# Kernel tuning notes

Measured on AMD Instinct MI355X. Metric: run time of the kernel, lower is better.

## Reference

```python
import jax, jax.numpy as jnp
import numpy as np

BS, SEQ, D, H = 2, 2048, 1024, 16
HD = D // H  # head_dim = 64


def setup_inputs() -> dict:
    key = jax.random.key(0)
    kx, kw = jax.random.split(key)
    x = jax.random.normal(kx, (BS, SEQ, D), dtype=jnp.float32)
    # qkv Linear: weight [3D, D] (xavier_normal), bias zeros
    std = float(np.sqrt(2.0 / (D + 3 * D)))
    W_qkv = jax.random.normal(kw, (3 * D, D), dtype=jnp.float32) * std
    b_qkv = jnp.zeros((3 * D,), dtype=jnp.float32)
    return {"x": x, "W_qkv": W_qkv, "b_qkv": b_qkv}


def reference(x, W_qkv, b_qkv):
    bs, seq_len, embed_dim = x.shape
    # fused QKV projection: [bs, seq, 3D]
    qkv = x @ W_qkv.T + b_qkv
    qkv = qkv.reshape(bs, seq_len, 3, H, HD)
    qkv = jnp.transpose(qkv, (2, 0, 3, 1, 4))  # [3, bs, H, seq, HD]
    Q, K, V = qkv[0], qkv[1], qkv[2]
    # past_kv is None -> total_len == seq_len, past_len == 0
    scores = jnp.einsum("bhqd,bhkd->bhqk", Q, K) / jnp.sqrt(jnp.float32(HD))
    # causal mask: True above diagonal -> -inf
    mask = jnp.triu(jnp.ones((seq_len, seq_len), dtype=bool), k=1)
    scores = jnp.where(mask[None, None, :, :], -jnp.inf, scores)
    probs = jax.nn.softmax(scores, axis=-1)
    # attn_dropout = 0.0 (eval) -> identity
    out = jnp.einsum("bhqk,bhkd->bhqd", probs, V)
    out = jnp.transpose(out, (0, 2, 1, 3)).reshape(bs, seq_len, embed_dim)
    return (out, (K, V))
```

## Files before the change

### kernel.cpp

```cpp
#include <hip/hip_runtime.h>

typedef __bf16 bf16_t;
typedef __bf16 bf16x8 __attribute__((ext_vector_type(8)));
typedef float f32x4 __attribute__((ext_vector_type(4)));
typedef unsigned long long u64;

__device__ __forceinline__ unsigned short bfbits(float f) {
  unsigned u = __float_as_uint(f);
  u += 0x7fffu + ((u >> 16) & 1u);
  return (unsigned short)(u >> 16);
}
__device__ __forceinline__ bf16_t f2bf(float f) {
  unsigned short s = bfbits(f);
  union { unsigned short s; bf16_t b; } cv; cv.s = s; return cv.b;
}

__device__ __forceinline__ void gl16(const void* g, void* l) {
  __builtin_amdgcn_global_load_lds(
      (const __attribute__((address_space(1))) void*)g,
      (__attribute__((address_space(3))) void*)l,
      16, 0, 0);
}

__global__ __launch_bounds__(256) void cvt_kernel(const float* __restrict__ x,
                                                  const float* __restrict__ Wf,
                                                  bf16_t* __restrict__ xb,
                                                  bf16_t* __restrict__ wb) {
  const int i = blockIdx.x * 256 + threadIdx.x;
  const float* src; bf16_t* dst; int j;
  if (i < 524288) { j = i; src = x; dst = xb; }
  else            { j = i - 524288; src = Wf; dst = wb; }
  const float4* s = (const float4*)src + (size_t)j * 2;
  float4 a = s[0], b = s[1];
  bf16x8 o;
  o[0] = f2bf(a.x); o[1] = f2bf(a.y); o[2] = f2bf(a.z); o[3] = f2bf(a.w);
  o[4] = f2bf(b.x); o[5] = f2bf(b.y); o[6] = f2bf(b.z); o[7] = f2bf(b.w);
  const int row = j >> 7, jr = j & 127;
  const int dstc = (row << 7) + (jr & ~3) + ((jr & 3) ^ ((row >> 1) & 3));
  *((bf16x8*)dst + dstc) = o;
}

#define GEMM_K 1024
__global__ __launch_bounds__(256) void qkv_gemm(
    const bf16_t* __restrict__ A,
    const bf16_t* __restrict__ B,
    const float* __restrict__ bias,
    float* __restrict__ Ko, float* __restrict__ Vo,
    bf16_t* __restrict__ Qb, bf16_t* __restrict__ Kb,
    bf16_t* __restrict__ Vt,
    int* __restrict__ qcnt)
{
  if (blockIdx.x == 0 && threadIdx.x == 0) *qcnt = 0;
  __shared__ bf16_t lsA[128 * 32];
  __shared__ bf16_t lsB[128 * 32];
  const int tid = threadIdx.x;
  const int lane = tid & 63;
  const int ln = lane & 15, qd = lane >> 4;
  const int wid = tid >> 6;
  const int wm = wid & 1, wn = wid >> 1;
  const int bm = blockIdx.x & 31, bn = blockIdx.x >> 5;
  const int m0 = bm * 128, n0 = bn * 128;
  const int qs = qd ^ ((ln >> 1) & 3);

  f32x4 acc[4][4] = {};

  const int c0 = tid, c1 = tid + 256;
  const bf16_t* ga0 = A + (size_t)(m0 + (c0 >> 2)) * GEMM_K + (c0 & 3) * 8;
  const bf16_t* ga1 = A + (size_t)(m0 + (c1 >> 2)) * GEMM_K + (c1 & 3) * 8;
  const bf16_t* gb0 = B + (size_t)(n0 + (c0 >> 2)) * GEMM_K + (c0 & 3) * 8;
  const bf16_t* gb1 = B + (size_t)(n0 + (c1 >> 2)) * GEMM_K + (c1 & 3) * 8;
  bf16_t* la0 = &lsA[c0 * 8];
  bf16_t* la1 = &lsA[c1 * 8];
  bf16_t* lb0 = &lsB[c0 * 8];
  bf16_t* lb1 = &lsB[c1 * 8];

  for (int k0 = 0; k0 < GEMM_K; k0 += 32) {
    __syncthreads();
    gl16(ga0 + k0, la0);
    gl16(ga1 + k0, la1);
    gl16(gb0 + k0, lb0);
    gl16(gb1 + k0, lb1);
    __syncthreads();
    bf16x8 af[4], bf[4];
#pragma unroll
    for (int mi = 0; mi < 4; ++mi)
      af[mi] = *(const bf16x8*)&lsA[(wm * 64 + mi * 16 + ln) * 32 + qs * 8];
#pragma unroll
    for (int ni = 0; ni < 4; ++ni)
      bf[ni] = *(const bf16x8*)&lsB[(wn * 64 + ni * 16 + ln) * 32 + qs * 8];
#pragma unroll
    for (int mi = 0; mi < 4; ++mi)
#pragma unroll
      for (int ni = 0; ni < 4; ++ni)
        acc[mi][ni] = __builtin_amdgcn_mfma_f32_16x16x32_bf16(af[mi], bf[ni], acc[mi][ni], 0, 0, 0);
  }

  const int sec = n0 >> 10;
#pragma unroll
  for (int mi = 0; mi < 4; ++mi) {
#pragma unroll
    for (int ni = 0; ni < 4; ++ni) {
      const int colg = n0 + wn * 64 + ni * 16 + ln;
      const float bv = bias[colg];
      const int cc = colg & 1023, h = cc >> 6, hd = cc & 63;
#pragma unroll
      for (int r = 0; r < 4; ++r) {
        const int mg = m0 + wm * 64 + mi * 16 + qd * 4 + r;
        const int b = mg >> 11, s = mg & 2047;
        const float val = acc[mi][ni][r] + bv;
        const int bhi = b * 16 + h;
        const size_t pidx = ((size_t)(bhi * 2048 + s)) * 64 + hd;
        const size_t sidx = (size_t)bhi * 131072 + (size_t)(s >> 6) * 4096 +
                            (size_t)(s & 63) * 64 + (((hd >> 3) ^ (s & 7)) << 3) + (hd & 7);
        if (sec == 0) {
          Qb[sidx] = f2bf(val * 0.18033688f);
        } else if (sec == 1) {
          Ko[pidx] = val;
          Kb[sidx] = f2bf(val);
        } else {
          Vo[pidx] = val;
          const size_t vidx = (size_t)bhi * 131072 + (size_t)(s >> 6) * 4096 +
                              (size_t)hd * 64 + ((((s >> 3) & 7) ^ (hd & 7)) << 3) + (s & 7);
          Vt[vidx] = f2bf(val);
        }
      }
    }
  }
}

__global__ __launch_bounds__(256) void attn_kernel(
    const bf16_t* __restrict__ Qb,
    const bf16_t* __restrict__ Kb,
    const bf16_t* __restrict__ Vt,
    float* __restrict__ Out,
    int* __restrict__ qcnt)
{
  __shared__ bf16_t lq[8192];
  __shared__ bf16_t lk[8192];
  __shared__ bf16_t lv[8192];
  __shared__ bf16_t lp[8192];
  __shared__ int task_sh;
  const int tid = threadIdx.x;
  const int lane = tid & 63, ln = lane & 15, qd = lane >> 4;
  const int w = tid >> 6;
  const int l7 = ln & 7;

  for (;;) {
    __syncthreads();
    if (tid == 0) task_sh = atomicAdd(qcnt, 1);
    __syncthreads();
    const int task = task_sh;
    if (task >= 512) break;
    const int it = (task < 256) ? (15 - (task >> 5)) : ((task - 256) >> 5);
    const int bh = task & 31;
    const int b = bh >> 4, h = bh & 15;

    const bf16_t* qbase = Qb + (size_t)bh * 131072 + (size_t)it * 8192;
    const bf16_t* kbase = Kb + (size_t)bh * 131072;
    const bf16_t* vbase = Vt + (size_t)bh * 131072;

#pragma unroll
    for (int i = 0; i < 4; ++i) {
      const int cc = tid + i * 256;
      gl16(qbase + cc * 8, &lq[cc * 8]);
      gl16(kbase + cc * 8, &lk[cc * 8]);
      gl16(vbase + cc * 8, &lv[cc * 8]);
    }
    __syncthreads();

    bf16x8 afq[2][2];
#pragma unroll
    for (int kk = 0; kk < 2; ++kk)
#pragma unroll
      for (int qi = 0; qi < 2; ++qi) {
        const int row = w * 32 + qi * 16 + ln;
        afq[kk][qi] = *(const bf16x8*)&lq[(row >> 6) * 4096 + (row & 63) * 64 +
                                          (((kk * 4 + qd) ^ l7) << 3)];
      }

    f32x4 oc[2][4] = {};
    float lsum[2] = {0.f, 0.f};
    const int qg = it * 128 + w * 32 + ln;

    for (int st = 0; st <= it; ++st) {
      if (st > 0) {
        __syncthreads();
#pragma unroll
        for (int i = 0; i < 4; ++i) {
          const int cc = tid + i * 256;
          gl16(kbase + (size_t)st * 8192 + cc * 8, &lk[cc * 8]);
          gl16(vbase + (size_t)st * 8192 + cc * 8, &lv[cc * 8]);
        }
        __syncthreads();
      }
      const bool diag = (st == it);

#pragma unroll
      for (int h2 = 0; h2 < 2; ++h2) {
        const int lofs = h2 * 4096;
        f32x4 sa[4][2] = {};
#pragma unroll
        for (int kk = 0; kk < 2; ++kk) {
          bf16x8 ak[4];
#pragma unroll
          for (int ki = 0; ki < 4; ++ki)
            ak[ki] = *(const bf16x8*)&lk[lofs + (ki * 16 + ln) * 64 + (((kk * 4 + qd) ^ l7) << 3)];
#pragma unroll
          for (int ki = 0; ki < 4; ++ki)
#pragma unroll
            for (int qi = 0; qi < 2; ++qi)
              sa[ki][qi] = __builtin_amdgcn_mfma_f32_16x16x32_bf16(ak[ki], afq[kk][qi], sa[ki][qi], 0, 0, 0);
        }

#pragma unroll
        for (int qi = 0; qi < 2; ++qi) {
          const int qgl = qg + qi * 16;
          const int q = w * 32 + qi * 16 + ln;
#pragma unroll
          for (int ki = 0; ki < 4; ++ki) {
            const int kb0 = (st * 2 + h2) * 64 + ki * 16 + qd * 4;
            float p0 = __builtin_amdgcn_exp2f(sa[ki][qi][0]);
            float p1 = __builtin_amdgcn_exp2f(sa[ki][qi][1]);
            float p2 = __builtin_amdgcn_exp2f(sa[ki][qi][2]);
            float p3 = __builtin_amdgcn_exp2f(sa[ki][qi][3]);
            if (diag) {
              if (kb0 + 0 > qgl) p0 = 0.f;
              if (kb0 + 1 > qgl) p1 = 0.f;
              if (kb0 + 2 > qgl) p2 = 0.f;
              if (kb0 + 3 > qgl) p3 = 0.f;
            }
            lsum[qi] += (p0 + p1) + (p2 + p3);
            const unsigned lo = (__float_as_uint(p1) & 0xFFFF0000u) | (__float_as_uint(p0) >> 16);
            const unsigned hi = (__float_as_uint(p3) & 0xFFFF0000u) | (__float_as_uint(p2) >> 16);
            const int g = (ki * 2 + (qd >> 1)) ^ l7;
            *(u64*)&lp[q * 64 + g * 8 + (qd & 1) * 4] = ((u64)hi << 32) | lo;
          }
        }

#pragma unroll
        for (int kk = 0; kk < 2; ++kk) {
          bf16x8 afp[2], bfv[4];
#pragma unroll
          for (int qi = 0; qi < 2; ++qi) {
            const int q = w * 32 + qi * 16 + ln;
            afp[qi] = *(const bf16x8*)&lp[q * 64 + (((kk * 4 + qd) ^ l7) << 3)];
          }
#pragma unroll
          for (int ni = 0; ni < 4; ++ni)
            bfv[ni] = *(const bf16x8*)&lv[lofs + (ni * 16 + ln) * 64 + (((kk * 4 + qd) ^ l7) << 3)];
#pragma unroll
          for (int qi = 0; qi < 2; ++qi)
#pragma unroll
            for (int ni = 0; ni < 4; ++ni)
              oc[qi][ni] = __builtin_amdgcn_mfma_f32_16x16x32_bf16(afp[qi], bfv[ni], oc[qi][ni], 0, 0, 0);
        }
      }
    }

    float lsq[2];
#pragma unroll
    for (int qi = 0; qi < 2; ++qi) {
      float ls = lsum[qi];
      ls += __shfl_xor(ls, 16);
      ls += __shfl_xor(ls, 32);
      lsq[qi] = ls;
    }
#pragma unroll
    for (int qi = 0; qi < 2; ++qi) {
#pragma unroll
      for (int r = 0; r < 4; ++r) {
        const float lval = __shfl(lsq[qi], qd * 4 + r);
        const float inv = 1.0f / lval;
        const int rowq = it * 128 + w * 32 + qi * 16 + qd * 4 + r;
#pragma unroll
        for (int ni = 0; ni < 4; ++ni) {
          const int colh = ni * 16 + ln;
          Out[(size_t)(b * 2048 + rowq) * 1024 + h * 64 + colh] = oc[qi][ni][r] * inv;
        }
      }
    }
  }
}

extern "C" void kernel_launch(void* const* d_in, const int* in_sizes, int n_in,
                              void* d_out, int out_size, void* d_ws, size_t ws_size,
                              hipStream_t stream) {
  const float* x = (const float*)d_in[0];
  const float* W = (const float*)d_in[1];
  const float* bq = (const float*)d_in[2];
  float* out = (float*)d_out;
  float* Ko = out + 4194304;
  float* Vo = out + 8388608;
  char* ws = (char*)d_ws;
  bf16_t* xb = (bf16_t*)ws;
  bf16_t* wb = (bf16_t*)(ws + 8388608);
  bf16_t* Qb = (bf16_t*)(ws + 14680064);
  bf16_t* Kb = (bf16_t*)(ws + 23068672);
  bf16_t* Vt = (bf16_t*)(ws + 31457280);
  int*    qcnt = (int*)(ws + 39845888);

  hipLaunchKernelGGL(cvt_kernel, dim3(3584), dim3(256), 0, stream, x, W, xb, wb);
  hipLaunchKernelGGL(qkv_gemm, dim3(768), dim3(256), 0, stream, xb, wb, bq, Ko, Vo, Qb, Kb, Vt, qcnt);
  hipLaunchKernelGGL(attn_kernel, dim3(512), dim3(256), 0, stream, Qb, Kb, Vt, out, qcnt);
}
```

Before: 182.0 us.

## Prefetch GEMM tiles via registers, remap blocks per XCD, pack V-transpose stores

The QKV GEMM now prefetches the next K-slice into registers while computing the current one, replacing direct global-to-LDS loads. Block indices are remapped so blocks on the same XCD share weight column tiles, improving L2 reuse. The V transposed bf16 output is written as one 64-bit store per four rows instead of four scalar stores, using truncation instead of round-to-nearest. This adds register pressure and slightly changes V rounding.

```diff
diff --git a/kernel.cpp b/kernel.cpp
--- a/kernel.cpp
+++ b/kernel.cpp
@@ -58,7 +58,10 @@
   const int ln = lane & 15, qd = lane >> 4;
   const int wid = tid >> 6;
   const int wm = wid & 1, wn = wid >> 1;
-  const int bm = blockIdx.x & 31, bn = blockIdx.x >> 5;
+  const int xcd = blockIdx.x & 7;
+  const int j = blockIdx.x >> 3;
+  const int bn = xcd * 3 + (j % 3);
+  const int bm = j / 3;
   const int m0 = bm * 128, n0 = bn * 128;
   const int qs = qd ^ ((ln >> 1) & 3);
 
@@ -69,18 +72,25 @@
   const bf16_t* ga1 = A + (size_t)(m0 + (c1 >> 2)) * GEMM_K + (c1 & 3) * 8;
   const bf16_t* gb0 = B + (size_t)(n0 + (c0 >> 2)) * GEMM_K + (c0 & 3) * 8;
   const bf16_t* gb1 = B + (size_t)(n0 + (c1 >> 2)) * GEMM_K + (c1 & 3) * 8;
-  bf16_t* la0 = &lsA[c0 * 8];
-  bf16_t* la1 = &lsA[c1 * 8];
-  bf16_t* lb0 = &lsB[c0 * 8];
-  bf16_t* lb1 = &lsB[c1 * 8];
+
+  float4 pa0 = *(const float4*)(ga0);
+  float4 pa1 = *(const float4*)(ga1);
+  float4 pb0 = *(const float4*)(gb0);
+  float4 pb1 = *(const float4*)(gb1);
 
   for (int k0 = 0; k0 < GEMM_K; k0 += 32) {
     __syncthreads();
-    gl16(ga0 + k0, la0);
-    gl16(ga1 + k0, la1);
-    gl16(gb0 + k0, lb0);
-    gl16(gb1 + k0, lb1);
-    __syncthreads();
+    *(float4*)&lsA[c0 * 8] = pa0;
+    *(float4*)&lsA[c1 * 8] = pa1;
+    *(float4*)&lsB[c0 * 8] = pb0;
+    *(float4*)&lsB[c1 * 8] = pb1;
+    __syncthreads();
+    if (k0 + 32 < GEMM_K) {
+      pa0 = *(const float4*)(ga0 + k0 + 32);
+      pa1 = *(const float4*)(ga1 + k0 + 32);
+      pb0 = *(const float4*)(gb0 + k0 + 32);
+      pb1 = *(const float4*)(gb1 + k0 + 32);
+    }
     bf16x8 af[4], bf[4];
 #pragma unroll
     for (int mi = 0; mi < 4; ++mi)
@@ -103,25 +113,38 @@
       const int colg = n0 + wn * 64 + ni * 16 + ln;
       const float bv = bias[colg];
       const int cc = colg & 1023, h = cc >> 6, hd = cc & 63;
-#pragma unroll
-      for (int r = 0; r < 4; ++r) {
-        const int mg = m0 + wm * 64 + mi * 16 + qd * 4 + r;
-        const int b = mg >> 11, s = mg & 2047;
-        const float val = acc[mi][ni][r] + bv;
-        const int bhi = b * 16 + h;
-        const size_t pidx = ((size_t)(bhi * 2048 + s)) * 64 + hd;
-        const size_t sidx = (size_t)bhi * 131072 + (size_t)(s >> 6) * 4096 +
-                            (size_t)(s & 63) * 64 + (((hd >> 3) ^ (s & 7)) << 3) + (hd & 7);
-        if (sec == 0) {
-          Qb[sidx] = f2bf(val * 0.18033688f);
-        } else if (sec == 1) {
-          Ko[pidx] = val;
-          Kb[sidx] = f2bf(val);
-        } else {
-          Vo[pidx] = val;
-          const size_t vidx = (size_t)bhi * 131072 + (size_t)(s >> 6) * 4096 +
-                              (size_t)hd * 64 + ((((s >> 3) & 7) ^ (hd & 7)) << 3) + (s & 7);
-          Vt[vidx] = f2bf(val);
+      if (sec == 2) {
+        unsigned u[4];
+#pragma unroll
+        for (int r = 0; r < 4; ++r) {
+          const int mg = m0 + wm * 64 + mi * 16 + qd * 4 + r;
+          const int b = mg >> 11, s = mg & 2047;
+          const float val = acc[mi][ni][r] + bv;
+          Vo[((size_t)((b * 16 + h) * 2048 + s)) * 64 + hd] = val;
+          u[r] = __float_as_uint(val);
+        }
+        const int mg0 = m0 + wm * 64 + mi * 16 + qd * 4;
+        const int b0 = mg0 >> 11, s0 = mg0 & 2047;
+        const unsigned lo = (u[1] & 0xFFFF0000u) | (u[0] >> 16);
+        const unsigned hi = (u[3] & 0xFFFF0000u) | (u[2] >> 16);
+        const size_t vb = (size_t)(b0 * 16 + h) * 131072 + (size_t)(s0 >> 6) * 4096 +
+                          (size_t)hd * 64 + ((((s0 >> 3) & 7) ^ (hd & 7)) << 3) + (s0 & 7);
+        *(u64*)&Vt[vb] = ((u64)hi << 32) | lo;
+      } else {
+#pragma unroll
+        for (int r = 0; r < 4; ++r) {
+          const int mg = m0 + wm * 64 + mi * 16 + qd * 4 + r;
+          const int b = mg >> 11, s = mg & 2047;
+          const float val = acc[mi][ni][r] + bv;
+          const int bhi = b * 16 + h;
+          const size_t sidx = (size_t)bhi * 131072 + (size_t)(s >> 6) * 4096 +
+                              (size_t)(s & 63) * 64 + (((hd >> 3) ^ (s & 7)) << 3) + (hd & 7);
+          if (sec == 0) {
+            Qb[sidx] = f2bf(val * 0.18033688f);
+          } else {
+            Ko[((size_t)(bhi * 2048 + s)) * 64 + hd] = val;
+            Kb[sidx] = f2bf(val);
+          }
         }
       }
     }
```

After: 180.0 us. Within noise of the previous version (-1.1%).
